# Kernel tuning notes

Hardware: AMD Instinct MI355X
Metric: run time of the kernel (lower is better)

Reference implementation:

```python
import jax, jax.numpy as jnp
import numpy as np

B, S, E, D, DE = 8, 128, 50, 300, 50  # batch, seq, edge_dim, gcn_dim, dep_embed_dim
EPS = 1e-6


def setup_inputs() -> dict:
    key = jax.random.key(0)
    ks = jax.random.split(key, 9)
    weight_prob_softmax = jax.nn.softmax(jax.random.normal(ks[0], (B, S, S, E)), axis=2)
    weight_adj = jax.random.normal(ks[1], (B, S, S, E))
    gcn_inputs = jax.random.normal(ks[2], (B, S, D))
    # self-loop added to adjacency after permute -> [B, E, S, S]; identity loops
    self_loop = jnp.broadcast_to(jnp.eye(S, dtype=jnp.float32), (B, E, S, S))
    W_w = jax.random.normal(ks[3], (D, D)) * 0.05          # gcn linear (in, out)
    W_b = jnp.zeros((D,))
    ln_a = jnp.ones((D,))
    ln_b = jnp.zeros((D,))
    refine_W = jax.random.normal(ks[4], (2 * D + 3 * E, DE)) * 0.05  # (750, 50)
    refine_b = jnp.zeros((DE,))
    return {
        "weight_prob_softmax": weight_prob_softmax,
        "weight_adj": weight_adj,
        "gcn_inputs": gcn_inputs,
        "self_loop": self_loop,
        "W_w": W_w, "W_b": W_b,
        "ln_a": ln_a, "ln_b": ln_b,
        "refine_W": refine_W, "refine_b": refine_b,
    }


def reference(weight_prob_softmax, weight_adj, gcn_inputs, self_loop,
              W_w, W_b, ln_a, ln_b, refine_W, refine_b):
    b, s, d = gcn_inputs.shape
    e = weight_prob_softmax.shape[-1]
    # [B,S,S,E] -> [B,E,S,S], add self loops
    wps = jnp.transpose(weight_prob_softmax, (0, 3, 1, 2)) + self_loop
    # per-relation-channel message passing: Ax[b,e,i,:] = sum_j wps[b,e,i,j] * x[b,j,:]
    Ax = jnp.einsum('beij,bjd->beid', wps, gcn_inputs)
    Ax = Ax.mean(axis=1)  # avg pooling over edge channels -> [B,S,D]
    h = Ax @ W_w + W_b
    # LayerNorm with unbiased std (torch x.std default) and (std + eps)
    mean = h.mean(axis=-1, keepdims=True)
    var_unbiased = jnp.sum((h - mean) ** 2, axis=-1, keepdims=True) / (d - 1)
    std = jnp.sqrt(var_unbiased)
    h = ln_a * (h - mean) / (std + EPS) + ln_b
    node = jax.nn.relu(h)  # [B,S,D]
    # node1[b,i,j] = node[b,j]; node2[b,i,j] = node[b,i]
    node1 = jnp.broadcast_to(node[:, None, :, :], (b, s, s, d))
    node2 = jnp.broadcast_to(node[:, :, None, :], (b, s, s, d))
    # diagonal edge features: [B,E,S] -> [B,S,E]
    diag = jnp.transpose(jnp.diagonal(weight_adj, axis1=1, axis2=2), (0, 2, 1))
    edge_i = jnp.broadcast_to(diag[:, None, :, :], (b, s, s, e))  # edge_i[b,i,j]=diag[b,j]
    edge_j = jnp.broadcast_to(diag[:, :, None, :], (b, s, s, e))  # edge_j[b,i,j]=diag[b,i]
    feat = jnp.concatenate([weight_adj, edge_i, edge_j, node1, node2], axis=-1)
    edge_out = feat @ refine_W + refine_b  # [B,S,S,DE]
    return node, edge_out
```

## Files before the change

kernel.cpp:

```cpp
#include <hip/hip_runtime.h>
#include <hip/hip_bf16.h>


typedef __bf16 bf16x8 __attribute__((ext_vector_type(8)));
typedef float f32x4 __attribute__((ext_vector_type(4)));

__device__ __forceinline__ unsigned short f2bf(float f) {
    __hip_bfloat16 h = __float2bfloat16(f);
    union { __hip_bfloat16 h; unsigned short u; } c; c.h = h; return c.u;
}

__global__ void __launch_bounds__(320) k_node(
    const float* __restrict__ wps,
    const float* __restrict__ x,
    const float* __restrict__ Ww,
    const float* __restrict__ Wb,
    const float* __restrict__ lna,
    const float* __restrict__ lnb,
    float* __restrict__ node_out)
{
    __shared__ float Ml[4][128];
    __shared__ float axm[4][304];
    __shared__ float hl[4][304];
    __shared__ float stats[8];
    int tid = threadIdx.x;
    int b = blockIdx.x >> 5;
    int ig = blockIdx.x & 31;
    int row0 = b * 128 + ig * 4;

    for (int slot = tid; slot < 512; slot += 320) {
        int r = slot >> 7, j = slot & 127;
        const float2* p = (const float2*)(wps + ((size_t)(row0 + r) * 128 + j) * 50);
        float s = 0.f;
#pragma unroll
        for (int n = 0; n < 25; ++n) { float2 v = p[n]; s += v.x + v.y; }
        Ml[r][j] = s * (1.0f / 50.0f) + (((ig * 4 + r) == j) ? 1.0f : 0.0f);
    }
    __syncthreads();

    if (tid < 300) {
        float a0 = 0.f, a1 = 0.f, a2 = 0.f, a3 = 0.f;
        const float* xp = x + (size_t)b * (128 * 300) + tid;
        for (int j = 0; j < 128; ++j) {
            float xv = xp[j * 300];
            a0 += Ml[0][j] * xv; a1 += Ml[1][j] * xv;
            a2 += Ml[2][j] * xv; a3 += Ml[3][j] * xv;
        }
        axm[0][tid] = a0; axm[1][tid] = a1; axm[2][tid] = a2; axm[3][tid] = a3;
    }
    __syncthreads();

    if (tid < 300) {
        float wb = Wb[tid];
        float h0 = wb, h1 = wb, h2 = wb, h3 = wb;
        const float* wp = Ww + tid;
        for (int k = 0; k < 300; ++k) {
            float w = wp[k * 300];
            h0 += axm[0][k] * w; h1 += axm[1][k] * w;
            h2 += axm[2][k] * w; h3 += axm[3][k] * w;
        }
        hl[0][tid] = h0; hl[1][tid] = h1; hl[2][tid] = h2; hl[3][tid] = h3;
    }
    __syncthreads();

    int wv = tid >> 6;
    if (wv < 4) {
        int lane = tid & 63;
        float s1 = 0.f, s2 = 0.f;
        for (int dd = lane; dd < 300; dd += 64) {
            float v = hl[wv][dd]; s1 += v; s2 += v * v;
        }
        for (int off = 32; off > 0; off >>= 1) {
            s1 += __shfl_down(s1, off);
            s2 += __shfl_down(s2, off);
        }
        if (lane == 0) {
            float mean = s1 * (1.0f / 300.0f);
            float var = (s2 - 300.0f * mean * mean) * (1.0f / 299.0f);
            var = fmaxf(var, 0.0f);
            stats[wv * 2] = mean;
            stats[wv * 2 + 1] = 1.0f / (sqrtf(var) + 1e-6f);
        }
    }
    __syncthreads();

    if (tid < 300) {
        float la = lna[tid];
        float lb = lnb[tid];
#pragma unroll
        for (int r = 0; r < 4; ++r) {
            float v = la * (hl[r][tid] - stats[r * 2]) * stats[r * 2 + 1] + lb;
            node_out[(size_t)(row0 + r) * 300 + tid] = fmaxf(v, 0.0f);
        }
    }
}

__global__ void k_r12(const float* __restrict__ wa,
                      const float* __restrict__ Rw,
                      const float* __restrict__ rb,
                      const float* __restrict__ node,
                      float* __restrict__ R1, float* __restrict__ R2)
{
    int wv = threadIdx.x >> 6;
    int k = threadIdx.x & 63;
    int row = blockIdx.x * 4 + wv;
    if (k >= 50) return;
    int b = row >> 7, s = row & 127;
    const float* dp = wa + (((size_t)(b * 128 + s)) * 128 + s) * 50;
    const float* np = node + (size_t)row * 300;
    float r1 = 0.f, r2 = rb[k];
    for (int e = 0; e < 50; ++e) {
        float de = dp[e];
        r1 += de * Rw[(50 + e) * 50 + k];
        r2 += de * Rw[(100 + e) * 50 + k];
    }
    for (int d = 0; d < 300; ++d) {
        float nv = np[d];
        r1 += nv * Rw[(150 + d) * 50 + k];
        r2 += nv * Rw[(450 + d) * 50 + k];
    }
    R1[row * 50 + k] = r1;
    R2[row * 50 + k] = r2;
}

__global__ void __launch_bounds__(256) k_edge(
    const float* __restrict__ wa,
    const float* __restrict__ Rw,
    const float* __restrict__ R1, const float* __restrict__ R2,
    float* __restrict__ eout)
{
    __shared__ __align__(16) unsigned short waA[128 * 72];
    __shared__ __align__(16) unsigned short rwBT[64 * 72];
    int tid = threadIdx.x;
    int bi = blockIdx.x;
    int b = bi >> 7;

    for (int idx = tid; idx < 2304; idx += 256) ((unsigned int*)rwBT)[idx] = 0u;
    for (int idx = tid; idx < 1408; idx += 256) {
        int j = idx / 11, c = idx % 11;
        *((unsigned int*)(waA + j * 72 + 50) + c) = 0u;
    }
    __syncthreads();

    const float2* wap = (const float2*)(wa + (size_t)bi * 6400);
    for (int idx = tid; idx < 3200; idx += 256) {
        float2 v = wap[idx];
        int f = idx * 2;
        int j = f / 50, e = f % 50;
        unsigned int pack = (unsigned int)f2bf(v.x) | ((unsigned int)f2bf(v.y) << 16);
        *(unsigned int*)(waA + j * 72 + e) = pack;
    }
    for (int idx = tid; idx < 2500; idx += 256) {
        int e = idx / 50, kk = idx % 50;
        rwBT[kk * 72 + e] = f2bf(Rw[idx]);
    }
    __syncthreads();

    int lane = tid & 63, wv = tid >> 6;
    int q = lane >> 4, lr = lane & 15;
    f32x4 acc[2][4] = {};

#pragma unroll
    for (int ks = 0; ks < 2; ++ks) {
        int e0 = ks * 32 + q * 8;
        bf16x8 a0 = *(const bf16x8*)&waA[(wv * 32 + lr) * 72 + e0];
        bf16x8 a1 = *(const bf16x8*)&waA[(wv * 32 + 16 + lr) * 72 + e0];
#pragma unroll
        for (int nt = 0; nt < 4; ++nt) {
            bf16x8 bb = *(const bf16x8*)&rwBT[(nt * 16 + lr) * 72 + e0];
            acc[0][nt] = __builtin_amdgcn_mfma_f32_16x16x32_bf16(a0, bb, acc[0][nt], 0, 0, 0);
            acc[1][nt] = __builtin_amdgcn_mfma_f32_16x16x32_bf16(a1, bb, acc[1][nt], 0, 0, 0);
        }
    }

    const float* r2p = R2 + (size_t)bi * 50;
    float* op = eout + (size_t)bi * 6400;
#pragma unroll
    for (int nt = 0; nt < 4; ++nt) {
        int kk = nt * 16 + lr;
        if (kk < 50) {
            float r2v = r2p[kk];
#pragma unroll
            for (int mi = 0; mi < 2; ++mi) {
                int jbase = wv * 32 + mi * 16 + q * 4;
#pragma unroll
                for (int r = 0; r < 4; ++r) {
                    int jj = jbase + r;
                    float v = acc[mi][nt][r] + R1[(size_t)(b * 128 + jj) * 50 + kk] + r2v;
                    op[(size_t)jj * 50 + kk] = v;
                }
            }
        }
    }
}

extern "C" void kernel_launch(void* const* d_in, const int* in_sizes, int n_in,
                              void* d_out, int out_size, void* d_ws, size_t ws_size,
                              hipStream_t stream)
{
    const float* wps = (const float*)d_in[0];
    const float* wa  = (const float*)d_in[1];
    const float* x   = (const float*)d_in[2];
    const float* Ww  = (const float*)d_in[4];
    const float* Wb  = (const float*)d_in[5];
    const float* lna = (const float*)d_in[6];
    const float* lnb = (const float*)d_in[7];
    const float* Rw  = (const float*)d_in[8];
    const float* rb  = (const float*)d_in[9];

    float* R1 = (float*)d_ws;
    float* R2 = ((float*)d_ws) + 51200;

    float* node_out = (float*)d_out;
    float* edge_out = node_out + 307200;

    k_node<<<256, 320, 0, stream>>>(wps, x, Ww, Wb, lna, lnb, node_out);
    k_r12 <<<256, 256, 0, stream>>>(wa, Rw, rb, node_out, R1, R2);
    k_edge<<<1024, 256, 0, stream>>>(wa, Rw, R1, R2, edge_out);
}
```

Before: 175.6 us.

## Fuse R1/R2 projection into node kernel and stage edge output through LDS

Folds the former k_r12 kernel into k_node, so each block computes its four rows' R1/R2 terms from the freshly computed node features and diagonal edge features held in shared memory, split over 8 partial groups and then reduced. The wps row reduction now stages coalesced float4 loads through a 50KB shared buffer instead of strided per-thread float2 reads, and the block size grows to 512. k_edge writes MFMA results to LDS and then emits float4-coalesced global stores with the R1 add, replacing scattered scalar stores. This removes one launch and the node round-trip, but the large LDS footprint may lower k_node occupancy.

```diff
diff --git a/kernel.cpp b/kernel.cpp
--- a/kernel.cpp
+++ b/kernel.cpp
@@ -10,37 +10,55 @@
     union { __hip_bfloat16 h; unsigned short u; } c; c.h = h; return c.u;
 }
 
-__global__ void __launch_bounds__(320) k_node(
+__global__ void __launch_bounds__(512) k_node(
     const float* __restrict__ wps,
+    const float* __restrict__ wa,
     const float* __restrict__ x,
     const float* __restrict__ Ww,
     const float* __restrict__ Wb,
     const float* __restrict__ lna,
     const float* __restrict__ lnb,
-    float* __restrict__ node_out)
+    const float* __restrict__ Rw,
+    const float* __restrict__ rb,
+    float* __restrict__ node_out,
+    float* __restrict__ R1, float* __restrict__ R2)
 {
+    __shared__ __align__(16) float stageF[12800];
     __shared__ float Ml[4][128];
     __shared__ float axm[4][304];
     __shared__ float hl[4][304];
+    __shared__ float diag[4][52];
     __shared__ float stats[8];
     int tid = threadIdx.x;
     int b = blockIdx.x >> 5;
     int ig = blockIdx.x & 31;
     int row0 = b * 128 + ig * 4;
 
-    for (int slot = tid; slot < 512; slot += 320) {
-        int r = slot >> 7, j = slot & 127;
-        const float2* p = (const float2*)(wps + ((size_t)(row0 + r) * 128 + j) * 50);
-        float s = 0.f;
-#pragma unroll
-        for (int n = 0; n < 25; ++n) { float2 v = p[n]; s += v.x + v.y; }
-        Ml[r][j] = s * (1.0f / 50.0f) + (((ig * 4 + r) == j) ? 1.0f : 0.0f);
-    }
-    __syncthreads();
+    const float4* wb4 = (const float4*)(wps + (size_t)row0 * 6400);
+    float4* s4 = (float4*)stageF;
+    for (int c = 0; c < 2; ++c) {
+        for (int i4 = tid; i4 < 3200; i4 += 512) s4[i4] = wb4[c * 3200 + i4];
+        __syncthreads();
+        if (tid < 256) {
+            int rl = tid >> 7, j = tid & 127;
+            const float* p = stageF + (rl * 128 + j) * 50;
+            float s = 0.f;
+#pragma unroll
+            for (int e = 0; e < 50; e += 2) s += p[e] + p[e + 1];
+            int r = c * 2 + rl;
+            Ml[r][j] = s * (1.0f / 50.0f) + (((ig * 4 + r) == j) ? 1.0f : 0.0f);
+        }
+        __syncthreads();
+    }
+    if (tid < 200) {
+        int r = tid / 50, e = tid % 50;
+        diag[r][e] = wa[(((size_t)(row0 + r)) * 128 + (ig * 4 + r)) * 50 + e];
+    }
 
     if (tid < 300) {
         float a0 = 0.f, a1 = 0.f, a2 = 0.f, a3 = 0.f;
-        const float* xp = x + (size_t)b * (128 * 300) + tid;
+        const float* xp = x + (size_t)b * 38400 + tid;
+#pragma unroll 4
         for (int j = 0; j < 128; ++j) {
             float xv = xp[j * 300];
             a0 += Ml[0][j] * xv; a1 += Ml[1][j] * xv;
@@ -54,6 +72,7 @@
         float wb = Wb[tid];
         float h0 = wb, h1 = wb, h2 = wb, h3 = wb;
         const float* wp = Ww + tid;
+#pragma unroll 4
         for (int k = 0; k < 300; ++k) {
             float w = wp[k * 300];
             h0 += axm[0][k] * w; h1 += axm[1][k] * w;
@@ -63,9 +82,8 @@
     }
     __syncthreads();
 
-    int wv = tid >> 6;
-    if (wv < 4) {
-        int lane = tid & 63;
+    if (tid < 256) {
+        int wv = tid >> 6, lane = tid & 63;
         float s1 = 0.f, s2 = 0.f;
         for (int dd = lane; dd < 300; dd += 64) {
             float v = hl[wv][dd]; s1 += v; s2 += v * v;
@@ -83,44 +101,51 @@
         }
     }
     __syncthreads();
-
     if (tid < 300) {
-        float la = lna[tid];
-        float lb = lnb[tid];
+        float la = lna[tid], lb = lnb[tid];
 #pragma unroll
         for (int r = 0; r < 4; ++r) {
             float v = la * (hl[r][tid] - stats[r * 2]) * stats[r * 2 + 1] + lb;
-            node_out[(size_t)(row0 + r) * 300 + tid] = fmaxf(v, 0.0f);
-        }
-    }
-}
-
-__global__ void k_r12(const float* __restrict__ wa,
-                      const float* __restrict__ Rw,
-                      const float* __restrict__ rb,
-                      const float* __restrict__ node,
-                      float* __restrict__ R1, float* __restrict__ R2)
-{
-    int wv = threadIdx.x >> 6;
-    int k = threadIdx.x & 63;
-    int row = blockIdx.x * 4 + wv;
-    if (k >= 50) return;
-    int b = row >> 7, s = row & 127;
-    const float* dp = wa + (((size_t)(b * 128 + s)) * 128 + s) * 50;
-    const float* np = node + (size_t)row * 300;
-    float r1 = 0.f, r2 = rb[k];
-    for (int e = 0; e < 50; ++e) {
-        float de = dp[e];
-        r1 += de * Rw[(50 + e) * 50 + k];
-        r2 += de * Rw[(100 + e) * 50 + k];
-    }
-    for (int d = 0; d < 300; ++d) {
-        float nv = np[d];
-        r1 += nv * Rw[(150 + d) * 50 + k];
-        r2 += nv * Rw[(450 + d) * 50 + k];
-    }
-    R1[row * 50 + k] = r1;
-    R2[row * 50 + k] = r2;
+            v = fmaxf(v, 0.0f);
+            node_out[(size_t)(row0 + r) * 300 + tid] = v;
+            axm[r][tid] = v;
+        }
+    }
+    __syncthreads();
+
+    if (tid < 400) {
+        int k = tid % 50, p = tid / 50;
+        float r1a[4] = {0.f, 0.f, 0.f, 0.f};
+        float r2a[4] = {0.f, 0.f, 0.f, 0.f};
+        int i0 = p * 44, i1 = (i0 + 44 < 350) ? i0 + 44 : 350;
+        for (int idx = i0; idx < i1; ++idx) {
+            float w1, w2;
+            if (idx < 50) { w1 = Rw[(50 + idx) * 50 + k]; w2 = Rw[(100 + idx) * 50 + k]; }
+            else { int d = idx - 50; w1 = Rw[(150 + d) * 50 + k]; w2 = Rw[(450 + d) * 50 + k]; }
+#pragma unroll
+            for (int r = 0; r < 4; ++r) {
+                float m = (idx < 50) ? diag[r][idx] : axm[r][idx - 50];
+                r1a[r] += m * w1; r2a[r] += m * w2;
+            }
+        }
+#pragma unroll
+        for (int r = 0; r < 4; ++r) {
+            stageF[p * 200 + r * 50 + k] = r1a[r];
+            stageF[1600 + p * 200 + r * 50 + k] = r2a[r];
+        }
+    }
+    __syncthreads();
+    if (tid < 200) {
+        int r = tid / 50, k = tid % 50;
+        float r1 = 0.f, r2 = rb[k];
+#pragma unroll
+        for (int p = 0; p < 8; ++p) {
+            r1 += stageF[p * 200 + r * 50 + k];
+            r2 += stageF[1600 + p * 200 + r * 50 + k];
+        }
+        R1[(size_t)(row0 + r) * 50 + k] = r1;
+        R2[(size_t)(row0 + r) * 50 + k] = r2;
+    }
 }
 
 __global__ void __launch_bounds__(256) k_edge(
@@ -129,8 +154,10 @@
     const float* __restrict__ R1, const float* __restrict__ R2,
     float* __restrict__ eout)
 {
-    __shared__ __align__(16) unsigned short waA[128 * 72];
-    __shared__ __align__(16) unsigned short rwBT[64 * 72];
+    __shared__ __align__(16) unsigned char smem[27648];
+    unsigned short* waA  = (unsigned short*)smem;
+    unsigned short* rwBT = (unsigned short*)(smem + 18432);
+    float* outF = (float*)smem;
     int tid = threadIdx.x;
     int bi = blockIdx.x;
     int b = bi >> 7;
@@ -172,9 +199,9 @@
             acc[1][nt] = __builtin_amdgcn_mfma_f32_16x16x32_bf16(a1, bb, acc[1][nt], 0, 0, 0);
         }
     }
+    __syncthreads();
 
     const float* r2p = R2 + (size_t)bi * 50;
-    float* op = eout + (size_t)bi * 6400;
 #pragma unroll
     for (int nt = 0; nt < 4; ++nt) {
         int kk = nt * 16 + lr;
@@ -184,13 +211,21 @@
             for (int mi = 0; mi < 2; ++mi) {
                 int jbase = wv * 32 + mi * 16 + q * 4;
 #pragma unroll
-                for (int r = 0; r < 4; ++r) {
-                    int jj = jbase + r;
-                    float v = acc[mi][nt][r] + R1[(size_t)(b * 128 + jj) * 50 + kk] + r2v;
-                    op[(size_t)jj * 50 + kk] = v;
-                }
+                for (int r = 0; r < 4; ++r)
+                    outF[(jbase + r) * 50 + kk] = acc[mi][nt][r] + r2v;
             }
         }
+    }
+    __syncthreads();
+
+    const float4* R1b = (const float4*)(R1 + (size_t)b * 6400);
+    const float4* L4  = (const float4*)outF;
+    float4* op4 = (float4*)(eout + (size_t)bi * 6400);
+    for (int f4 = tid; f4 < 1600; f4 += 256) {
+        float4 v = L4[f4];
+        float4 r = R1b[f4];
+        v.x += r.x; v.y += r.y; v.z += r.z; v.w += r.w;
+        op4[f4] = v;
     }
 }
 
@@ -214,7 +249,7 @@
     float* node_out = (float*)d_out;
     float* edge_out = node_out + 307200;
 
-    k_node<<<256, 320, 0, stream>>>(wps, x, Ww, Wb, lna, lnb, node_out);
-    k_r12 <<<256, 256, 0, stream>>>(wa, Rw, rb, node_out, R1, R2);
+    k_node<<<256, 512, 0, stream>>>(wps, wa, x, Ww, Wb, lna, lnb, Rw, rb,
+                                    node_out, R1, R2);
     k_edge<<<1024, 256, 0, stream>>>(wa, Rw, R1, R2, edge_out);
 }
```

New measurement: 184.3 us. 1.05x slower.
